# Kernel tuning notes

Measured on AMD Instinct MI355X. Metric: run time of the kernel, lower is better.

## Reference

```python
import jax, jax.numpy as jnp
import numpy as np

N = 32768          # n_atoms
E = 524288         # n_edges (avg degree 16)
MUL = 8            # multiplicity of 0e and 1o in irreps_in/out
NB = 8             # n_basis
HR = 64            # hidden_radial
NTP = 4 * MUL * MUL  # tensor-product weight_numel (4 CG paths)
AVG_NEI = 16.0
INV_SQRT3 = 1.0 / np.sqrt(3.0)      # w3j(1,1,0) component
ALPHA = 1.0 / np.sqrt(2.0 * MUL)    # path normalization: fan_in = 2 paths * mul_in*mul_sh


def setup_inputs() -> dict:
    key = jax.random.key(0)
    ks = jax.random.split(key, 12)
    h = jax.random.normal(ks[0], (N, 4 * MUL), jnp.float32)            # [N, 8 scalars + 8*3 vectors]
    edge_index = jax.random.randint(ks[1], (2, E), 0, N)               # [2, E] int
    edge_sh = jax.random.normal(ks[2], (E, 4), jnp.float32)            # [E, 1x0e + 1x1o]
    edge_radial = jax.random.uniform(ks[3], (E, NB), jnp.float32)      # [E, n_basis]

    def lin(k, fi, fo):
        return (jax.random.normal(k, (fi, fo), jnp.float32) / np.sqrt(fi)).astype(jnp.float32)

    W1 = lin(ks[4], NB, HR); b1 = jnp.zeros((HR,), jnp.float32)
    W2 = lin(ks[5], HR, HR); b2 = jnp.zeros((HR,), jnp.float32)
    W3 = lin(ks[6], HR, NTP); b3 = jnp.zeros((NTP,), jnp.float32)
    Ws = jax.random.normal(ks[7], (MUL, MUL), jnp.float32)             # self-interaction, scalar block
    Wv = jax.random.normal(ks[8], (MUL, MUL), jnp.float32)             # self-interaction, vector block
    return dict(h=h, edge_index=edge_index, edge_sh=edge_sh, edge_radial=edge_radial,
                n_atoms=N, W1=W1, b1=b1, W2=W2, b2=b2, W3=W3, b3=b3, Ws=Ws, Wv=Wv)


def reference(h, edge_index, edge_sh, edge_radial, n_atoms, W1, b1, W2, b2, W3, b3, Ws, Wv):
    src, dst = edge_index[0], edge_index[1]

    # radial MLP -> per-edge tensor-product weights [E, 256]
    x = jax.nn.silu(edge_radial @ W1 + b1)
    x = jax.nn.silu(x @ W2 + b2)
    tpw = x @ W3 + b3
    P = MUL * MUL
    W00  = tpw[:, 0 * P:1 * P].reshape(-1, MUL, MUL)  # 0e x 0e -> 0e
    W110 = tpw[:, 1 * P:2 * P].reshape(-1, MUL, MUL)  # 1o x 1o -> 0e (dot)
    W01  = tpw[:, 2 * P:3 * P].reshape(-1, MUL, MUL)  # 0e x 1o -> 1o
    W10  = tpw[:, 3 * P:4 * P].reshape(-1, MUL, MUL)  # 1o x 0e -> 1o

    hs = h[:, :MUL]                         # [N, 8] scalars
    hv = h[:, MUL:].reshape(-1, MUL, 3)     # [N, 8, 3] vectors
    hs_e = hs[src]                          # gather [E, 8]
    hv_e = hv[src]                          # gather [E, 8, 3]
    sh0 = edge_sh[:, 0]                     # [E]
    sh1 = edge_sh[:, 1:4]                   # [E, 3]

    # equivariant tensor product (e3nn FullyConnectedTensorProduct, l<=1)
    m0 = ALPHA * (jnp.einsum('eu,euw->ew', hs_e * sh0[:, None], W00)
                  + INV_SQRT3 * jnp.einsum('eui,ei,euw->ew', hv_e, sh1, W110))       # [E, 8]
    m1 = ALPHA * (jnp.einsum('eu,ei,euw->ewi', hs_e, sh1, W01)
                  + jnp.einsum('eui,euw->ewi', hv_e * sh0[:, None, None], W10))      # [E, 8, 3]
    messages = jnp.concatenate([m0, m1.reshape(-1, 3 * MUL)], axis=-1)               # [E, 32]

    # scatter-add to destination nodes, degree normalization
    agg = jax.ops.segment_sum(messages, dst, num_segments=n_atoms) / np.sqrt(AVG_NEI)

    # self interaction (o3.Linear: block-diagonal per irrep, 1/sqrt(fan_in))
    self0 = (hs @ Ws) / np.sqrt(MUL)
    self1 = jnp.einsum('nui,uw->nwi', hv, Wv) / np.sqrt(MUL)
    h_self = jnp.concatenate([self0, self1.reshape(-1, 3 * MUL)], axis=-1)

    return h_self + agg
```

## Files before the change

### kernel.cpp

```cpp
#include <hip/hip_runtime.h>

#define N_ATOMS 32768
#define E_EDGES 524288
#define FEAT 32
#define TPB 512
#define WPB 8
#define PASSES 8
#define GRID (E_EDGES / (WPB * PASSES * 16))
#define INV_SQRT3 0.57735026919f
#define MSG_SCALE 0.0625f
#define SELF_SCALE 0.35355339059f

#define WS_MSG   0
#define WS_CNT   33554432
#define WS_CUR   33685504
#define WS_OFFS  33816576
#define WS_BSUM  33947648
#define WS_BBASE 33948160
#define WS_EIDS  33948672

typedef __bf16 bf16;
typedef _Float16 f16;
typedef __attribute__((ext_vector_type(8))) __bf16 bf16x8;
typedef __attribute__((ext_vector_type(4))) float f32x4;
typedef __attribute__((ext_vector_type(2))) _Float16 f16x2;
typedef __attribute__((ext_vector_type(4))) _Float16 f16x4;

__device__ __forceinline__ float silu(float x) { return x / (1.0f + __expf(-x)); }

__device__ __forceinline__ f32x4 mfma16(bf16x8 a, bf16x8 b, f32x4 c) {
    return __builtin_amdgcn_mfma_f32_16x16x32_bf16(a, b, c, 0, 0, 0);
}

__global__ __launch_bounds__(256) void count_kernel(const int* __restrict__ eidx,
                                                    int* __restrict__ cnt) {
    int e = blockIdx.x * 256 + threadIdx.x;
    atomicAdd(&cnt[eidx[E_EDGES + e]], 1);
}

__global__ __launch_bounds__(256) void scan1_kernel(const int* __restrict__ cnt,
                                                    int* __restrict__ bsum) {
    __shared__ int s[256];
    int t = threadIdx.x;
    s[t] = cnt[blockIdx.x * 256 + t];
    __syncthreads();
    for (int d = 128; d > 0; d >>= 1) {
        if (t < d) s[t] += s[t + d];
        __syncthreads();
    }
    if (t == 0) bsum[blockIdx.x] = s[0];
}

__global__ __launch_bounds__(64) void scan2_kernel(const int* __restrict__ bsum,
                                                   int* __restrict__ bbase) {
    int lane = threadIdx.x;
    int v0 = bsum[2 * lane], v1 = bsum[2 * lane + 1];
    int s = v0 + v1, x = s;
    for (int d = 1; d < 64; d <<= 1) {
        int y = __shfl_up(x, d, 64);
        if (lane >= d) x += y;
    }
    int excl = x - s;
    bbase[2 * lane] = excl;
    bbase[2 * lane + 1] = excl + v0;
}

__global__ __launch_bounds__(256) void scan3_kernel(const int* __restrict__ cnt,
                                                    const int* __restrict__ bbase,
                                                    int* __restrict__ offs) {
    int t = threadIdx.x, lane = t & 63, w = t >> 6;
    int v = cnt[blockIdx.x * 256 + t];
    int x = v;
    for (int d = 1; d < 64; d <<= 1) {
        int y = __shfl_up(x, d, 64);
        if (lane >= d) x += y;
    }
    __shared__ int wsum[4];
    if (lane == 63) wsum[w] = x;
    __syncthreads();
    int base = bbase[blockIdx.x];
    for (int i = 0; i < w; ++i) base += wsum[i];
    offs[blockIdx.x * 256 + t] = base + x - v;
}

__global__ __launch_bounds__(256) void fill_kernel(const int* __restrict__ eidx,
                                                   const int* __restrict__ offs,
                                                   int* __restrict__ cur,
                                                   int* __restrict__ eids) {
    int e = blockIdx.x * 256 + threadIdx.x;
    int d = eidx[E_EDGES + e];
    int slot = atomicAdd(&cur[d], 1);
    eids[offs[d] + slot] = e;
}

__global__ __launch_bounds__(TPB, 4) void edge_kernel(
    const float* __restrict__ h, const int* __restrict__ eidx,
    const float* __restrict__ esh, const float* __restrict__ erad,
    const float* __restrict__ W1, const float* __restrict__ b1,
    const float* __restrict__ W2, const float* __restrict__ b2,
    const float* __restrict__ W3, const float* __restrict__ b3,
    f16* __restrict__ msg)
{
    __shared__ bf16x8 w1f[4 * 64];
    __shared__ bf16x8 w2f[2 * 4 * 64];
    __shared__ bf16x8 w3f[2 * 16 * 64];
    __shared__ float b1s[64], b2s[64], b3s[256];
    __shared__ __align__(16) char xtp[WPB][16 * 66 * 4];

    const int tid = threadIdx.x;

    {
        bf16* p = (bf16*)w1f;
        for (int f = tid; f < 4 * 64 * 8; f += TPB) {
            int n0 = f >> 9, lane = (f >> 3) & 63, j = f & 7;
            int k = ((lane >> 4) << 3) + j, n = (n0 << 4) + (lane & 15);
            p[f] = (k < 8) ? (bf16)W1[k * 64 + n] : (bf16)0.0f;
        }
        p = (bf16*)w2f;
        for (int f = tid; f < 2 * 4 * 64 * 8; f += TPB) {
            int kk = f >> 11, n0 = (f >> 9) & 3, lane = (f >> 3) & 63, j = f & 7;
            int k = (kk << 5) + ((lane >> 4) << 3) + j, n = (n0 << 4) + (lane & 15);
            p[f] = (bf16)W2[k * 64 + n];
        }
        p = (bf16*)w3f;
        for (int f = tid; f < 2 * 16 * 64 * 8; f += TPB) {
            int kk = f >> 13, n0 = (f >> 9) & 15, lane = (f >> 3) & 63, j = f & 7;
            int k = (kk << 5) + ((lane >> 4) << 3) + j, n = (n0 << 4) + (lane & 15);
            p[f] = (bf16)W3[k * 256 + n];
        }
        if (tid < 64) { b1s[tid] = b1[tid]; b2s[tid] = b2[tid]; }
        if (tid < 256) b3s[tid] = b3[tid];
    }
    __syncthreads();

    const int wave = tid >> 6, lane = tid & 63;
    const int g = lane >> 4, m = lane & 15;
    const int me = lane >> 2, w0 = (lane & 3) * 2;

    bf16* xs = (bf16*)&xtp[wave][0];
    float* tp = (float*)&xtp[wave][0];

    for (int pass = 0; pass < PASSES; ++pass) {
        const int tile = (blockIdx.x * WPB + wave) * PASSES + pass;
        const int e0 = tile * 16;

        const int src = eidx[e0 + me];
        const float4 shv = *(const float4*)(esh + (long)(e0 + me) * 4);
        float hrow[32];
        {
            const float* hp = h + (long)src * FEAT;
#pragma unroll
            for (int c4 = 0; c4 < 8; ++c4)
                ((float4*)hrow)[c4] = ((const float4*)hp)[c4];
        }

        bf16x8 arad;
        {
            float r[8] = {0.f, 0.f, 0.f, 0.f, 0.f, 0.f, 0.f, 0.f};
            if (g == 0) {
                const float4* rp = (const float4*)(erad + (long)(e0 + m) * 8);
                float4 r0 = rp[0], r1 = rp[1];
                r[0] = r0.x; r[1] = r0.y; r[2] = r0.z; r[3] = r0.w;
                r[4] = r1.x; r[5] = r1.y; r[6] = r1.z; r[7] = r1.w;
            }
#pragma unroll
            for (int j = 0; j < 8; ++j) arad[j] = (bf16)r[j];
        }

#pragma unroll
        for (int n0 = 0; n0 < 4; ++n0) {
            f32x4 acc = {};
            acc = mfma16(arad, w1f[n0 * 64 + lane], acc);
            float bn = b1s[n0 * 16 + m];
#pragma unroll
            for (int q = 0; q < 4; ++q) {
                float v = silu(acc[q] + bn);
                xs[(g * 4 + q) * 72 + n0 * 16 + m] = (bf16)v;
            }
        }
        bf16x8 a2[2];
        a2[0] = *(const bf16x8*)(xs + m * 72 + g * 8);
        a2[1] = *(const bf16x8*)(xs + m * 72 + 32 + g * 8);

#pragma unroll
        for (int n0 = 0; n0 < 4; ++n0) {
            f32x4 acc = {};
            acc = mfma16(a2[0], w2f[n0 * 64 + lane], acc);
            acc = mfma16(a2[1], w2f[(4 + n0) * 64 + lane], acc);
            float bn = b2s[n0 * 16 + m];
#pragma unroll
            for (int q = 0; q < 4; ++q) {
                float v = silu(acc[q] + bn);
                xs[(g * 4 + q) * 72 + n0 * 16 + m] = (bf16)v;
            }
        }
        bf16x8 a3[2];
        a3[0] = *(const bf16x8*)(xs + m * 72 + g * 8);
        a3[1] = *(const bf16x8*)(xs + m * 72 + 32 + g * 8);

        float m0a0 = 0.f, m0a1 = 0.f, s20 = 0.f, s21 = 0.f;
        float sv[6] = {0.f, 0.f, 0.f, 0.f, 0.f, 0.f};

#pragma unroll
        for (int c = 0; c < 4; ++c) {
#pragma unroll
            for (int n0 = 0; n0 < 4; ++n0) {
                f32x4 acc = {};
                acc = mfma16(a3[0], w3f[(c * 4 + n0) * 64 + lane], acc);
                acc = mfma16(a3[1], w3f[(16 + c * 4 + n0) * 64 + lane], acc);
                float bn = b3s[c * 64 + n0 * 16 + m];
#pragma unroll
                for (int q = 0; q < 4; ++q)
                    tp[(g * 4 + q) * 66 + n0 * 16 + m] = acc[q] + bn;
            }
#pragma unroll
            for (int u = 0; u < 8; ++u) {
                float2 t = *(const float2*)(tp + me * 66 + u * 8 + w0);
                if (c == 0) {
                    float a0 = hrow[u] * shv.x;
                    m0a0 += a0 * t.x; m0a1 += a0 * t.y;
                } else if (c == 1) {
                    float a1 = INV_SQRT3 * (hrow[8 + u * 3] * shv.y +
                                            hrow[9 + u * 3] * shv.z +
                                            hrow[10 + u * 3] * shv.w);
                    m0a0 += a1 * t.x; m0a1 += a1 * t.y;
                } else if (c == 2) {
                    s20 += hrow[u] * t.x; s21 += hrow[u] * t.y;
                } else {
                    sv[0] += hrow[8 + u * 3] * t.x;
                    sv[1] += hrow[9 + u * 3] * t.x;
                    sv[2] += hrow[10 + u * 3] * t.x;
                    sv[3] += hrow[8 + u * 3] * t.y;
                    sv[4] += hrow[9 + u * 3] * t.y;
                    sv[5] += hrow[10 + u * 3] * t.y;
                }
            }
        }

        f16* row = msg + (long)(e0 + me) * FEAT;
        f16x2 p0;
        p0[0] = (f16)(MSG_SCALE * m0a0);
        p0[1] = (f16)(MSG_SCALE * m0a1);
        *(f16x2*)(row + w0) = p0;
        f16 m1v[6];
#pragma unroll
        for (int i = 0; i < 3; ++i) {
            float s1i = (i == 0) ? shv.y : (i == 1) ? shv.z : shv.w;
            m1v[i]     = (f16)(MSG_SCALE * (s1i * s20 + shv.x * sv[i]));
            m1v[3 + i] = (f16)(MSG_SCALE * (s1i * s21 + shv.x * sv[3 + i]));
        }
        f16* rp = row + 8 + 3 * w0;
        { f16x2 t; t[0] = m1v[0]; t[1] = m1v[1]; *(f16x2*)(rp)     = t; }
        { f16x2 t; t[0] = m1v[2]; t[1] = m1v[3]; *(f16x2*)(rp + 2) = t; }
        { f16x2 t; t[0] = m1v[4]; t[1] = m1v[5]; *(f16x2*)(rp + 4) = t; }
    }
}

__global__ __launch_bounds__(256) void gather_kernel(
    const f16* __restrict__ msg, const int* __restrict__ eids,
    const int* __restrict__ offs, const int* __restrict__ cnt,
    const float* __restrict__ h,
    const float* __restrict__ Ws, const float* __restrict__ Wv,
    float* __restrict__ out)
{
    const int t = threadIdx.x;
    const int n = blockIdx.x * 32 + (t >> 3);
    const int L = t & 7;
    const int base = offs[n], deg = cnt[n];

    float a0 = 0.f, a1 = 0.f, a2 = 0.f, a3 = 0.f;
    for (int i = 0; i < deg; ++i) {
        int eid = eids[base + i];
        f16x4 v = *(const f16x4*)(msg + (long)eid * FEAT + L * 4);
        a0 += (float)v[0]; a1 += (float)v[1]; a2 += (float)v[2]; a3 += (float)v[3];
    }

    const float* hrow = h + (long)n * FEAT;
    const int f0 = L * 4;
    float o[4];
    if (L < 2) {
#pragma unroll
        for (int j = 0; j < 4; ++j) {
            int w = f0 + j;
            float a = 0.f;
#pragma unroll
            for (int u = 0; u < 8; ++u) a += hrow[u] * Ws[u * 8 + w];
            o[j] = SELF_SCALE * a;
        }
    } else {
#pragma unroll
        for (int j = 0; j < 4; ++j) {
            int f = f0 + j, w = (f - 8) / 3, i3 = (f - 8) % 3;
            float a = 0.f;
#pragma unroll
            for (int u = 0; u < 8; ++u) a += hrow[8 + u * 3 + i3] * Wv[u * 8 + w];
            o[j] = SELF_SCALE * a;
        }
    }
    float4 r;
    r.x = o[0] + a0; r.y = o[1] + a1; r.z = o[2] + a2; r.w = o[3] + a3;
    *(float4*)(out + (long)n * FEAT + f0) = r;
}

extern "C" void kernel_launch(void* const* d_in, const int* in_sizes, int n_in,
                              void* d_out, int out_size, void* d_ws, size_t ws_size,
                              hipStream_t stream)
{
    const float* h    = (const float*)d_in[0];
    const int*   eidx = (const int*)  d_in[1];
    const float* esh  = (const float*)d_in[2];
    const float* erad = (const float*)d_in[3];
    const float* W1   = (const float*)d_in[5];
    const float* b1   = (const float*)d_in[6];
    const float* W2   = (const float*)d_in[7];
    const float* b2   = (const float*)d_in[8];
    const float* W3   = (const float*)d_in[9];
    const float* b3   = (const float*)d_in[10];
    const float* Ws   = (const float*)d_in[11];
    const float* Wv   = (const float*)d_in[12];
    float* out = (float*)d_out;

    char* ws = (char*)d_ws;
    f16* msg   = (f16*)(ws + WS_MSG);
    int* cnt   = (int*)(ws + WS_CNT);
    int* cur   = (int*)(ws + WS_CUR);
    int* offs  = (int*)(ws + WS_OFFS);
    int* bsum  = (int*)(ws + WS_BSUM);
    int* bbase = (int*)(ws + WS_BBASE);
    int* eids  = (int*)(ws + WS_EIDS);

    hipMemsetAsync(cnt, 0, 2 * N_ATOMS * sizeof(int), stream);

    count_kernel<<<E_EDGES / 256, 256, 0, stream>>>(eidx, cnt);
    scan1_kernel<<<N_ATOMS / 256, 256, 0, stream>>>(cnt, bsum);
    scan2_kernel<<<1, 64, 0, stream>>>(bsum, bbase);
    scan3_kernel<<<N_ATOMS / 256, 256, 0, stream>>>(cnt, bbase, offs);
    edge_kernel<<<GRID, TPB, 0, stream>>>(h, eidx, esh, erad,
                                          W1, b1, W2, b2, W3, b3, msg);
    fill_kernel<<<E_EDGES / 256, 256, 0, stream>>>(eidx, offs, cur, eids);
    gather_kernel<<<N_ATOMS / 32, 256, 0, stream>>>(msg, eids, offs, cnt,
                                                    h, Ws, Wv, out);
}
```

Baseline: 171.3 us.

## Prepack MLP weights once in a prep kernel and read fragments from global

Adds a small prep kernel that converts W1/W2/W3 to bf16 in MFMA fragment order once, so the edge kernel no longer rebuilds them in shared memory per block. Dropping those shared arrays lowers LDS use, which allows more blocks per CU (launch bounds raised to 6) and fewer passes per wave (more, smaller blocks). The weight fragments are now read from global/L2 on every use instead of LDS, which may add load latency in the MLP inner loop.

```diff
diff --git a/kernel.cpp b/kernel.cpp
--- a/kernel.cpp
+++ b/kernel.cpp
@@ -5,7 +5,7 @@
 #define FEAT 32
 #define TPB 512
 #define WPB 8
-#define PASSES 8
+#define PASSES 2
 #define GRID (E_EDGES / (WPB * PASSES * 16))
 #define INV_SQRT3 0.57735026919f
 #define MSG_SCALE 0.0625f
@@ -18,6 +18,7 @@
 #define WS_BSUM  33947648
 #define WS_BBASE 33948160
 #define WS_EIDS  33948672
+#define WS_WF    36045824
 
 typedef __bf16 bf16;
 typedef _Float16 f16;
@@ -30,6 +31,31 @@
 
 __device__ __forceinline__ f32x4 mfma16(bf16x8 a, bf16x8 b, f32x4 c) {
     return __builtin_amdgcn_mfma_f32_16x16x32_bf16(a, b, c, 0, 0, 0);
+}
+
+__global__ __launch_bounds__(256) void prep_kernel(
+    const float* __restrict__ W1, const float* __restrict__ W2,
+    const float* __restrict__ W3, bf16* __restrict__ wf)
+{
+    int idx = blockIdx.x * 256 + threadIdx.x;
+    float v;
+    if (idx < 2048) {
+        int f = idx;
+        int n0 = f >> 9, lane = (f >> 3) & 63, j = f & 7;
+        int k = ((lane >> 4) << 3) + j, n = (n0 << 4) + (lane & 15);
+        v = (k < 8) ? W1[k * 64 + n] : 0.0f;
+    } else if (idx < 6144) {
+        int f = idx - 2048;
+        int kk = f >> 11, n0 = (f >> 9) & 3, lane = (f >> 3) & 63, j = f & 7;
+        int k = (kk << 5) + ((lane >> 4) << 3) + j, n = (n0 << 4) + (lane & 15);
+        v = W2[k * 64 + n];
+    } else {
+        int f = idx - 6144;
+        int kk = f >> 13, n0 = (f >> 9) & 15, lane = (f >> 3) & 63, j = f & 7;
+        int k = (kk << 5) + ((lane >> 4) << 3) + j, n = (n0 << 4) + (lane & 15);
+        v = W3[k * 256 + n];
+    }
+    wf[idx] = (bf16)v;
 }
 
 __global__ __launch_bounds__(256) void count_kernel(const int* __restrict__ eidx,
@@ -93,45 +119,25 @@
     eids[offs[d] + slot] = e;
 }
 
-__global__ __launch_bounds__(TPB, 4) void edge_kernel(
+__global__ __launch_bounds__(TPB, 6) void edge_kernel(
     const float* __restrict__ h, const int* __restrict__ eidx,
     const float* __restrict__ esh, const float* __restrict__ erad,
-    const float* __restrict__ W1, const float* __restrict__ b1,
-    const float* __restrict__ W2, const float* __restrict__ b2,
-    const float* __restrict__ W3, const float* __restrict__ b3,
+    const bf16* __restrict__ wf,
+    const float* __restrict__ b1, const float* __restrict__ b2,
+    const float* __restrict__ b3,
     f16* __restrict__ msg)
 {
-    __shared__ bf16x8 w1f[4 * 64];
-    __shared__ bf16x8 w2f[2 * 4 * 64];
-    __shared__ bf16x8 w3f[2 * 16 * 64];
     __shared__ float b1s[64], b2s[64], b3s[256];
     __shared__ __align__(16) char xtp[WPB][16 * 66 * 4];
 
     const int tid = threadIdx.x;
-
-    {
-        bf16* p = (bf16*)w1f;
-        for (int f = tid; f < 4 * 64 * 8; f += TPB) {
-            int n0 = f >> 9, lane = (f >> 3) & 63, j = f & 7;
-            int k = ((lane >> 4) << 3) + j, n = (n0 << 4) + (lane & 15);
-            p[f] = (k < 8) ? (bf16)W1[k * 64 + n] : (bf16)0.0f;
-        }
-        p = (bf16*)w2f;
-        for (int f = tid; f < 2 * 4 * 64 * 8; f += TPB) {
-            int kk = f >> 11, n0 = (f >> 9) & 3, lane = (f >> 3) & 63, j = f & 7;
-            int k = (kk << 5) + ((lane >> 4) << 3) + j, n = (n0 << 4) + (lane & 15);
-            p[f] = (bf16)W2[k * 64 + n];
-        }
-        p = (bf16*)w3f;
-        for (int f = tid; f < 2 * 16 * 64 * 8; f += TPB) {
-            int kk = f >> 13, n0 = (f >> 9) & 15, lane = (f >> 3) & 63, j = f & 7;
-            int k = (kk << 5) + ((lane >> 4) << 3) + j, n = (n0 << 4) + (lane & 15);
-            p[f] = (bf16)W3[k * 256 + n];
-        }
-        if (tid < 64) { b1s[tid] = b1[tid]; b2s[tid] = b2[tid]; }
-        if (tid < 256) b3s[tid] = b3[tid];
-    }
+    if (tid < 64) { b1s[tid] = b1[tid]; b2s[tid] = b2[tid]; }
+    if (tid < 256) b3s[tid] = b3[tid];
     __syncthreads();
+
+    const bf16x8* w1f = (const bf16x8*)(wf);
+    const bf16x8* w2f = (const bf16x8*)(wf + 2048);
+    const bf16x8* w3f = (const bf16x8*)(wf + 6144);
 
     const int wave = tid >> 6, lane = tid & 63;
     const int g = lane >> 4, m = lane & 15;
@@ -328,15 +334,17 @@
     int* bsum  = (int*)(ws + WS_BSUM);
     int* bbase = (int*)(ws + WS_BBASE);
     int* eids  = (int*)(ws + WS_EIDS);
+    bf16* wf   = (bf16*)(ws + WS_WF);
 
     hipMemsetAsync(cnt, 0, 2 * N_ATOMS * sizeof(int), stream);
 
+    prep_kernel<<<88, 256, 0, stream>>>(W1, W2, W3, wf);
     count_kernel<<<E_EDGES / 256, 256, 0, stream>>>(eidx, cnt);
     scan1_kernel<<<N_ATOMS / 256, 256, 0, stream>>>(cnt, bsum);
     scan2_kernel<<<1, 64, 0, stream>>>(bsum, bbase);
     scan3_kernel<<<N_ATOMS / 256, 256, 0, stream>>>(cnt, bbase, offs);
-    edge_kernel<<<GRID, TPB, 0, stream>>>(h, eidx, esh, erad,
-                                          W1, b1, W2, b2, W3, b3, msg);
+    edge_kernel<<<GRID, TPB, 0, stream>>>(h, eidx, esh, erad, wf,
+                                          b1, b2, b3, msg);
     fill_kernel<<<E_EDGES / 256, 256, 0, stream>>>(eidx, offs, cur, eids);
     gather_kernel<<<N_ATOMS / 32, 256, 0, stream>>>(msg, eids, offs, cnt,
                                                     h, Ws, Wv, out);
```

Measured after the change: 419.7 us. 145% more time.
